# Kernel optimization log

Measured on AMD Instinct MI355X. Metric: run time of the kernel, lower is better.

Reference implementation:

```python
import jax
import jax.numpy as jnp
from jax import lax
import numpy as np

D_MODEL = 768
D_INNER = 1536  # d_model * expand_factor
D_STATE = 16
D_CONV = 4
BATCH = 2
SEQ = 2048
EPS = 1e-5


def silu(x):
    return x * jax.nn.sigmoid(x)


def setup_inputs() -> dict:
    key = jax.random.key(0)
    ks = jax.random.split(key, 24)
    n = lambda k, shape, s=0.1: jax.random.normal(k, shape, dtype=jnp.float32) * s
    inp = {
        "x": jax.random.normal(ks[0], (BATCH, SEQ, D_MODEL), dtype=jnp.float32),
        "ln_g": jnp.ones((D_MODEL,), jnp.float32),
        "ln_b": jnp.zeros((D_MODEL,), jnp.float32),
        "W_in": n(ks[1], (D_INNER, D_MODEL)),
        "b_in": n(ks[2], (D_INNER,)),
        "conv_w": n(ks[3], (D_INNER, 1, D_CONV), 0.02),
        "conv_b": jnp.zeros((D_INNER,), jnp.float32),
        "W_A": n(ks[4], (D_STATE, D_INNER)),
        "b_A": n(ks[5], (D_STATE,)),
        "W_B": n(ks[6], (D_STATE, D_INNER)),
        "b_B": n(ks[7], (D_STATE,)),
        "W_C": n(ks[8], (D_STATE, D_INNER)),
        "b_C": n(ks[9], (D_STATE,)),
        "W_dt": n(ks[10], (D_STATE, D_INNER)),
        "b_dt": n(ks[11], (D_STATE,)),
        "W_S": n(ks[12], (2 * D_INNER, D_INNER)),
        "b_S": n(ks[13], (2 * D_INNER,)),
        "W_gate": n(ks[14], (D_INNER, D_MODEL)),
        "b_gate": n(ks[15], (D_INNER,)),
        "W_out": n(ks[16], (D_MODEL, D_INNER)),
        "b_out": n(ks[17], (D_MODEL,)),
    }
    return inp


def reference(x, ln_g, ln_b, W_in, b_in, conv_w, conv_b, W_A, b_A, W_B, b_B,
              W_C, b_C, W_dt, b_dt, W_S, b_S, W_gate, b_gate, W_out, b_out):
    residual = x
    # LayerNorm
    mu = jnp.mean(x, axis=-1, keepdims=True)
    var = jnp.mean((x - mu) ** 2, axis=-1, keepdims=True)
    xn = (x - mu) * lax.rsqrt(var + EPS) * ln_g + ln_b
    # in projection -> [B, S, D_INNER]
    xp = xn @ W_in.T + b_in
    # depthwise causal conv1d over time
    k = conv_w.shape[-1]
    xc = jnp.moveaxis(xp, 1, 2)  # [B, D, L]
    xc = lax.conv_general_dilated(
        xc, conv_w, window_strides=(1,), padding=[(k - 1, 0)],
        dimension_numbers=("NCH", "OIH", "NCH"),
        feature_group_count=xc.shape[1])
    xc = xc + conv_b[None, :, None]
    xa = silu(jnp.moveaxis(xc, 1, 2))  # [B, S, D]
    # selective gating of SSM input (S_b computed but unused, as in source)
    S = xa @ W_S.T + b_S
    d = xa.shape[-1]
    S_a = jax.nn.sigmoid(S[..., :d])
    u = xa * S_a  # [B, S, D]
    # input-dependent SSM params [B, S, N]
    A = -jnp.exp(u @ W_A.T + b_A)
    dt = jnp.exp(u @ W_dt.T + b_dt)
    Bm = u @ W_B.T + b_B
    Cm = u @ W_C.T + b_C
    decay = jnp.exp(A * dt)  # [B, S, N]

    def step(h, inputs):
        dec_t, B_t, C_t, u_t = inputs  # [B,N],[B,N],[B,N],[B,D]
        h = h * dec_t[:, None, :] + B_t[:, None, :] * u_t[:, :, None]  # [B,D,N]
        y = jnp.einsum("bdn,bn->bd", h, C_t)
        return h, y

    h0 = jnp.zeros((u.shape[0], u.shape[2], decay.shape[-1]), u.dtype)
    scan_in = (jnp.moveaxis(decay, 1, 0), jnp.moveaxis(Bm, 1, 0),
               jnp.moveaxis(Cm, 1, 0), jnp.moveaxis(u, 1, 0))
    _, ys = lax.scan(step, h0, scan_in)
    y = jnp.moveaxis(ys, 0, 1)  # [B, S, D]
    # output gating + projection + residual
    gate = silu(xn @ W_gate.T + b_gate)
    out = (gate * y) @ W_out.T + b_out + residual
    return out
```

## Files before the change

### kernel.cpp

```cpp
#include <hip/hip_runtime.h>


typedef unsigned short u16;
using short8 = __attribute__((ext_vector_type(8))) short;
using f32x4  = __attribute__((ext_vector_type(4))) float;

#define BATCH 2
#define SEQ   2048
#define DM    768
#define DI    1536
#define NIG   (2*DI)
#define NST   16
#define LCH   64
#define NCH   32
#define NTOK  (BATCH*SEQ)

__device__ __forceinline__ u16 f2b(float x) {
  unsigned u = __float_as_uint(x);
  u += 0x7FFFu + ((u >> 16) & 1u);
  return (u16)(u >> 16);
}
__device__ __forceinline__ float b2f(u16 v) { return __uint_as_float((unsigned)v << 16); }
__device__ __forceinline__ float sigmoidf_(float x) { return 1.f / (1.f + expf(-x)); }
__device__ __forceinline__ float siluf_(float x) { return x / (1.f + expf(-x)); }

__global__ __launch_bounds__(256) void cast_bf16(const float* __restrict__ in, u16* __restrict__ out, int n4) {
  int i = blockIdx.x * 256 + threadIdx.x;
  if (i >= n4) return;
  float4 v = ((const float4*)in)[i];
  ushort4 o; o.x = f2b(v.x); o.y = f2b(v.y); o.z = f2b(v.z); o.w = f2b(v.w);
  ((ushort4*)out)[i] = o;
}

__global__ __launch_bounds__(256) void cast_ingate(const float* __restrict__ Wi, const float* __restrict__ Wg,
                                                   const float* __restrict__ bi, const float* __restrict__ bg,
                                                   u16* __restrict__ Wb, float* __restrict__ bias) {
  int i = blockIdx.x * 256 + threadIdx.x;
  if (i >= NIG * DM) return;
  int r = i / DM, c = i % DM;
  Wb[i] = f2b(r < DI ? Wi[(size_t)r * DM + c] : Wg[(size_t)(r - DI) * DM + c]);
  if (i < NIG) bias[i] = (i < DI) ? bi[i] : bg[i - DI];
}

__global__ __launch_bounds__(256) void cast_wabcd(const float* __restrict__ WA, const float* __restrict__ Wdt,
                                                  const float* __restrict__ WB, const float* __restrict__ WC,
                                                  const float* __restrict__ bA, const float* __restrict__ bdt,
                                                  const float* __restrict__ bB, const float* __restrict__ bC,
                                                  u16* __restrict__ Wb, float* __restrict__ bias64) {
  int i = blockIdx.x * 256 + threadIdx.x;
  if (i >= 64 * DI) return;
  int r = i / DI, c = i % DI;
  const float* src = (r < 16) ? WA + (size_t)r * DI
                  : (r < 32) ? Wdt + (size_t)(r - 16) * DI
                  : (r < 48) ? WB + (size_t)(r - 32) * DI
                             : WC + (size_t)(r - 48) * DI;
  Wb[i] = f2b(src[c]);
  if (i < 64) bias64[i] = (i < 16) ? bA[i] : (i < 32) ? bdt[i - 16] : (i < 48) ? bB[i - 32] : bC[i - 48];
}

__global__ __launch_bounds__(256) void ln_kernel(const float* __restrict__ x, const float* __restrict__ g,
                                                 const float* __restrict__ bb, u16* __restrict__ xn) {
  int m = blockIdx.x, tid = threadIdx.x;
  const float* xr = x + (size_t)m * DM;
  float v0 = xr[tid], v1 = xr[tid + 256], v2 = xr[tid + 512];
  float s  = v0 + v1 + v2;
  float s2 = fmaf(v0, v0, fmaf(v1, v1, v2 * v2));
  #pragma unroll
  for (int off = 32; off > 0; off >>= 1) { s += __shfl_down(s, off); s2 += __shfl_down(s2, off); }
  __shared__ float sh[8];
  int wave = tid >> 6, lane = tid & 63;
  if (lane == 0) { sh[wave] = s; sh[4 + wave] = s2; }
  __syncthreads();
  float S1 = sh[0] + sh[1] + sh[2] + sh[3];
  float S2 = sh[4] + sh[5] + sh[6] + sh[7];
  float mu = S1 * (1.f / DM);
  float var = S2 * (1.f / DM) - mu * mu;
  float rs = rsqrtf(var + 1e-5f);
  u16* o = xn + (size_t)m * DM;
  o[tid]       = f2b((v0 - mu) * rs * g[tid]       + bb[tid]);
  o[tid + 256] = f2b((v1 - mu) * rs * g[tid + 256] + bb[tid + 256]);
  o[tid + 512] = f2b((v2 - mu) * rs * g[tid + 512] + bb[tid + 512]);
}

__device__ __forceinline__ void gll16(const void* g, void* l) {
  __builtin_amdgcn_global_load_lds((const __attribute__((address_space(1))) void*)g,
                                   (__attribute__((address_space(3))) void*)l, 16, 0, 0);
}

template <int MODE>
__global__ __launch_bounds__(512) void gemm_bt(const u16* __restrict__ A, const u16* __restrict__ B,
                                               const float* __restrict__ bias, const float* __restrict__ aux,
                                               const u16* __restrict__ auxb,
                                               float* __restrict__ C, u16* __restrict__ Cb,
                                               int M, int N, int K) {
  __shared__ __align__(16) u16 As[4][128 * 32];
  __shared__ __align__(16) u16 Bs[4][128 * 32];
  const int tid = threadIdx.x, wave = tid >> 6, lane = tid & 63;

  const int nbx = gridDim.x, nwg = nbx * gridDim.y;
  const int orig = blockIdx.y * nbx + blockIdx.x;
  const int cpx = nwg >> 3;
  const int swz = (orig & 7) * cpx + (orig >> 3);
  const int m0 = (swz / nbx) * 128, n0 = (swz % nbx) * 128;

  const int wm = (wave >> 1) * 32, wn = (wave & 1) * 64;
  const int fr = lane & 15, fq = lane >> 4;
  f32x4 acc[2][4] = {};

  const int c0 = tid;
  const u16* Ag0 = A + (size_t)(m0 + (c0 >> 2)) * K + ((c0 & 3) ^ ((c0 >> 3) & 3)) * 8;
  const u16* Bg0 = B + (size_t)(n0 + (c0 >> 2)) * K + ((c0 & 3) ^ ((c0 >> 3) & 3)) * 8;
  const int lofs = (wave * 64) * 8;

  int offA[2], offB[4];
  #pragma unroll
  for (int i = 0; i < 2; ++i) {
    int ra = wm + i * 16 + fr;
    offA[i] = ra * 32 + (fq ^ ((ra >> 1) & 3)) * 8;
  }
  #pragma unroll
  for (int i = 0; i < 4; ++i) {
    int rb = wn + i * 16 + fr;
    offB[i] = rb * 32 + (fq ^ ((rb >> 1) & 3)) * 8;
  }

  const int nk = K >> 5;

#define STAGE_BT(tt) { gll16(Ag0 + (tt) * 32, (u16*)As[(tt) & 3] + lofs); \
                       gll16(Bg0 + (tt) * 32, (u16*)Bs[(tt) & 3] + lofs); }
#define COMPUTE_BT(tt) { const u16* as_ = As[(tt) & 3]; const u16* bs_ = Bs[(tt) & 3]; \
    short8 av[2], bv[4]; \
    _Pragma("unroll") for (int i = 0; i < 2; ++i) av[i] = *(const short8*)(as_ + offA[i]); \
    _Pragma("unroll") for (int i = 0; i < 4; ++i) bv[i] = *(const short8*)(bs_ + offB[i]); \
    _Pragma("unroll") for (int mi = 0; mi < 2; ++mi) \
      _Pragma("unroll") for (int ni = 0; ni < 4; ++ni) \
        acc[mi][ni] = __builtin_amdgcn_mfma_f32_16x16x32_bf16(av[mi], bv[ni], acc[mi][ni], 0, 0, 0); }

  STAGE_BT(0); STAGE_BT(1); STAGE_BT(2);

  for (int t = 0; t < nk - 3; ++t) {
    asm volatile("s_waitcnt vmcnt(4)" ::: "memory");
    __builtin_amdgcn_s_barrier();
    STAGE_BT(t + 3);
    COMPUTE_BT(t);
  }
  asm volatile("s_waitcnt vmcnt(4)" ::: "memory");
  __builtin_amdgcn_s_barrier();
  COMPUTE_BT(nk - 3);
  asm volatile("s_waitcnt vmcnt(2)" ::: "memory");
  __builtin_amdgcn_s_barrier();
  COMPUTE_BT(nk - 2);
  asm volatile("s_waitcnt vmcnt(0)" ::: "memory");
  __builtin_amdgcn_s_barrier();
  COMPUTE_BT(nk - 1);
#undef STAGE_BT
#undef COMPUTE_BT

  #pragma unroll
  for (int ni = 0; ni < 4; ++ni) {
    int col = n0 + wn + ni * 16 + fr;
    float bv_ = bias[col];
    #pragma unroll
    for (int mi = 0; mi < 2; ++mi) {
      int row = m0 + wm + mi * 16 + fq * 4;
      #pragma unroll
      for (int j = 0; j < 4; ++j) {
        size_t off = (size_t)(row + j) * N + col;
        float z = acc[mi][ni][j] + bv_;
        if (MODE == 0) {
          C[off] = z + aux[off];
        } else if (MODE == 1) {
          Cb[off] = f2b(b2f(auxb[off]) * sigmoidf_(z));
        } else {
          Cb[off] = f2b(z);
        }
      }
    }
  }
}

__global__ __launch_bounds__(256) void gemm_abcd(const u16* __restrict__ A, const u16* __restrict__ B,
                                                 float* __restrict__ Zp, int M, int K) {
  __shared__ __align__(16) u16 As[2][64 * 64];
  __shared__ __align__(16) u16 Bs[2][64 * 64];
  const int tid = threadIdx.x, wave = tid >> 6, lane = tid & 63;
  const int m0 = blockIdx.x * 64;
  const int ks = blockIdx.y;
  const int Kq = K >> 2;
  const int kbase = ks * Kq;
  const int wm = wave * 16;
  const int fr = lane & 15, fq = lane >> 4;
  f32x4 acc[4] = {};

  const int c0 = tid, c1 = tid + 256;
  const u16* Ag0 = A + (size_t)(m0 + (c0 >> 3)) * K + kbase + ((c0 & 7) ^ ((c0 >> 3) & 7)) * 8;
  const u16* Ag1 = A + (size_t)(m0 + (c1 >> 3)) * K + kbase + ((c1 & 7) ^ ((c1 >> 3) & 7)) * 8;
  const u16* Bg0 = B + (size_t)(c0 >> 3) * K + kbase + ((c0 & 7) ^ ((c0 >> 3) & 7)) * 8;
  const u16* Bg1 = B + (size_t)(c1 >> 3) * K + kbase + ((c1 & 7) ^ ((c1 >> 3) & 7)) * 8;
  const int lo0 = (wave * 64) * 8;
  const int lo1 = (256 + wave * 64) * 8;

  int offAv[2], offBv[2][4];
  {
    int r = wm + fr;
    #pragma unroll
    for (int kk = 0; kk < 2; ++kk) offAv[kk] = r * 64 + ((kk * 4 + fq) ^ (r & 7)) * 8;
    #pragma unroll
    for (int i = 0; i < 4; ++i) {
      int rb = i * 16 + fr;
      #pragma unroll
      for (int kk = 0; kk < 2; ++kk) offBv[kk][i] = rb * 64 + ((kk * 4 + fq) ^ (rb & 7)) * 8;
    }
  }

  const int nk = Kq >> 6;
  gll16(Ag0, (u16*)As[0] + lo0);
  gll16(Ag1, (u16*)As[0] + lo1);
  gll16(Bg0, (u16*)Bs[0] + lo0);
  gll16(Bg1, (u16*)Bs[0] + lo1);

  for (int t = 0; t < nk; ++t) {
    __syncthreads();
    if (t + 1 < nk) {
      int ko = (t + 1) * 64;
      gll16(Ag0 + ko, (u16*)As[(t + 1) & 1] + lo0);
      gll16(Ag1 + ko, (u16*)As[(t + 1) & 1] + lo1);
      gll16(Bg0 + ko, (u16*)Bs[(t + 1) & 1] + lo0);
      gll16(Bg1 + ko, (u16*)Bs[(t + 1) & 1] + lo1);
    }
    const u16* as = As[t & 1];
    const u16* bs = Bs[t & 1];
    #pragma unroll
    for (int kk = 0; kk < 2; ++kk) {
      short8 av = *(const short8*)(as + offAv[kk]);
      short8 bv[4];
      #pragma unroll
      for (int i = 0; i < 4; ++i) bv[i] = *(const short8*)(bs + offBv[kk][i]);
      #pragma unroll
      for (int ni = 0; ni < 4; ++ni)
        acc[ni] = __builtin_amdgcn_mfma_f32_16x16x32_bf16(av, bv[ni], acc[ni], 0, 0, 0);
    }
  }

  float* zp = Zp + (size_t)ks * M * 64;
  #pragma unroll
  for (int ni = 0; ni < 4; ++ni) {
    int col = ni * 16 + fr;
    #pragma unroll
    for (int j = 0; j < 4; ++j) {
      int row = m0 + wm + fq * 4 + j;
      zp[(size_t)row * 64 + col] = acc[ni][j];
    }
  }
}

__global__ __launch_bounds__(256) void abcd_combine(const float* __restrict__ Zp, const float* __restrict__ bias64,
                                                    float* __restrict__ dec, float* __restrict__ Bm,
                                                    float* __restrict__ Cm, int M) {
  int idx = blockIdx.x * 256 + threadIdx.x;
  int row = idx >> 4, n = idx & 15;
  float zA = bias64[n], zDt = bias64[16 + n], zB = bias64[32 + n], zC = bias64[48 + n];
  #pragma unroll
  for (int ks = 0; ks < 4; ++ks) {
    const float* zp = Zp + ((size_t)ks * M + row) * 64;
    zA += zp[n]; zDt += zp[16 + n]; zB += zp[32 + n]; zC += zp[48 + n];
  }
  size_t o = (size_t)row * NST + n;
  dec[o] = expf(-expf(zA + zDt));
  Bm[o] = zB;
  Cm[o] = zC;
}

__global__ __launch_bounds__(256) void conv_silu(const u16* __restrict__ xpg, const float* __restrict__ cw,
                                                 const float* __restrict__ cb, u16* __restrict__ xab) {
  int idx = blockIdx.x * 256 + threadIdx.x;
  int d8 = idx % (DI / 8);
  int token = idx / (DI / 8);
  int t = token % SEQ;
  int d0 = d8 * 8;
  const short8* xv = (const short8*)(xpg + (size_t)token * NIG + d0);
  short8 z8 = {0, 0, 0, 0, 0, 0, 0, 0};
  short8 x3 = (t >= 3) ? xv[-3 * (NIG / 8)] : z8;
  short8 x2 = (t >= 2) ? xv[-2 * (NIG / 8)] : z8;
  short8 x1 = (t >= 1) ? xv[-1 * (NIG / 8)] : z8;
  short8 x0 = xv[0];
  const float4* cw4 = (const float4*)cw;
  float4 cbl = ((const float4*)cb)[d8 * 2], cbh = ((const float4*)cb)[d8 * 2 + 1];
  float cbv[8] = {cbl.x, cbl.y, cbl.z, cbl.w, cbh.x, cbh.y, cbh.z, cbh.w};
  short8 o;
  #pragma unroll
  for (int j = 0; j < 8; ++j) {
    float4 w = cw4[d0 + j];
    float a = cbv[j];
    a = fmaf(b2f((u16)x3[j]), w.x, a);
    a = fmaf(b2f((u16)x2[j]), w.y, a);
    a = fmaf(b2f((u16)x1[j]), w.z, a);
    a = fmaf(b2f((u16)x0[j]), w.w, a);
    o[j] = (short)f2b(siluf_(a));
  }
  *(short8*)(xab + (size_t)token * DI + d0) = o;
}

__global__ __launch_bounds__(256) void scan_phase1(const u16* __restrict__ ub, const float* __restrict__ dec,
                                                   const float* __restrict__ Bm, float* __restrict__ lend,
                                                   float* __restrict__ P) {
  __shared__ float dl[LCH * NST], bl[LCH * NST];
  int bid = blockIdx.x;
  int dblk = bid % 6, b = (bid / 6) % BATCH, c = bid / (6 * BATCH);
  int d = dblk * 256 + threadIdx.x;
  int t0 = c * LCH;
  size_t base16 = (size_t)(b * SEQ + t0) * NST;
  for (int i = threadIdx.x; i < LCH * NST; i += 256) { dl[i] = dec[base16 + i]; bl[i] = Bm[base16 + i]; }
  __syncthreads();
  float h[NST];
  #pragma unroll
  for (int n = 0; n < NST; ++n) h[n] = 0.f;
  const u16* up = ub + (size_t)(b * SEQ + t0) * DI + d;
  for (int t = 0; t < LCH; ++t) {
    float uu = b2f(up[(size_t)t * DI]);
    #pragma unroll
    for (int n = 0; n < NST; ++n) h[n] = fmaf(h[n], dl[t * NST + n], bl[t * NST + n] * uu);
  }
  float* lo = lend + ((size_t)(c * BATCH + b) * DI + d) * NST;
  ((float4*)lo)[0] = make_float4(h[0], h[1], h[2], h[3]);
  ((float4*)lo)[1] = make_float4(h[4], h[5], h[6], h[7]);
  ((float4*)lo)[2] = make_float4(h[8], h[9], h[10], h[11]);
  ((float4*)lo)[3] = make_float4(h[12], h[13], h[14], h[15]);
  if (dblk == 0 && threadIdx.x < NST) {
    float pr = 1.f;
    for (int t = 0; t < LCH; ++t) pr *= dl[t * NST + threadIdx.x];
    P[(size_t)(c * BATCH + b) * NST + threadIdx.x] = pr;
  }
}

__global__ __launch_bounds__(256) void scan_phase2(const float* __restrict__ lend, const float* __restrict__ P,
                                                   float* __restrict__ Hin) {
  int flat = blockIdx.x * 256 + threadIdx.x;
  int n = flat & 15;
  int d = (flat >> 4) % DI;
  int b = flat / (DI * NST);
  float h = 0.f;
  for (int c = 0; c < NCH; ++c) {
    size_t idx = ((size_t)(c * BATCH + b) * DI + d) * NST + n;
    Hin[idx] = h;
    h = fmaf(P[(size_t)(c * BATCH + b) * NST + n], h, lend[idx]);
  }
}

__global__ __launch_bounds__(256) void scan_phase3(const u16* __restrict__ ub, const float* __restrict__ dec,
                                                   const float* __restrict__ Bm, const float* __restrict__ Cm,
                                                   const float* __restrict__ Hin, const u16* __restrict__ xpg,
                                                   u16* __restrict__ gy) {
  __shared__ float dl[LCH * NST], bl[LCH * NST], cl[LCH * NST];
  int bid = blockIdx.x;
  int dblk = bid % 6, b = (bid / 6) % BATCH, c = bid / (6 * BATCH);
  int d = dblk * 256 + threadIdx.x;
  int t0 = c * LCH;
  size_t base16 = (size_t)(b * SEQ + t0) * NST;
  for (int i = threadIdx.x; i < LCH * NST; i += 256) {
    dl[i] = dec[base16 + i]; bl[i] = Bm[base16 + i]; cl[i] = Cm[base16 + i];
  }
  __syncthreads();
  float h[NST];
  const float4* hi = (const float4*)(Hin + ((size_t)(c * BATCH + b) * DI + d) * NST);
  float4 h0 = hi[0], h1 = hi[1], h2 = hi[2], h3 = hi[3];
  h[0]=h0.x; h[1]=h0.y; h[2]=h0.z; h[3]=h0.w; h[4]=h1.x; h[5]=h1.y; h[6]=h1.z; h[7]=h1.w;
  h[8]=h2.x; h[9]=h2.y; h[10]=h2.z; h[11]=h2.w; h[12]=h3.x; h[13]=h3.y; h[14]=h3.z; h[15]=h3.w;
  const u16* up = ub + (size_t)(b * SEQ + t0) * DI + d;
  const u16* gp = xpg + (size_t)(b * SEQ + t0) * NIG + DI + d;
  u16* yp = gy + (size_t)(b * SEQ + t0) * DI + d;
  for (int t = 0; t < LCH; ++t) {
    float uu = b2f(up[(size_t)t * DI]);
    float acc = 0.f;
    #pragma unroll
    for (int n = 0; n < NST; ++n) {
      h[n] = fmaf(h[n], dl[t * NST + n], bl[t * NST + n] * uu);
      acc = fmaf(h[n], cl[t * NST + n], acc);
    }
    float g = b2f(gp[(size_t)t * NIG]);
    yp[(size_t)t * DI] = f2b(siluf_(g) * acc);
  }
}

extern "C" void kernel_launch(void* const* d_in, const int* in_sizes, int n_in,
                              void* d_out, int out_size, void* d_ws, size_t ws_size,
                              hipStream_t stream) {
  const float* x      = (const float*)d_in[0];
  const float* ln_g   = (const float*)d_in[1];
  const float* ln_b   = (const float*)d_in[2];
  const float* W_in   = (const float*)d_in[3];
  const float* b_in   = (const float*)d_in[4];
  const float* conv_w = (const float*)d_in[5];
  const float* conv_b = (const float*)d_in[6];
  const float* W_A    = (const float*)d_in[7];
  const float* b_A    = (const float*)d_in[8];
  const float* W_B    = (const float*)d_in[9];
  const float* b_B    = (const float*)d_in[10];
  const float* W_C    = (const float*)d_in[11];
  const float* b_C    = (const float*)d_in[12];
  const float* W_dt   = (const float*)d_in[13];
  const float* b_dt   = (const float*)d_in[14];
  const float* W_S    = (const float*)d_in[15];
  const float* b_S    = (const float*)d_in[16];
  const float* W_gate = (const float*)d_in[17];
  const float* b_gate = (const float*)d_in[18];
  const float* W_out  = (const float*)d_in[19];
  const float* b_out  = (const float*)d_in[20];
  float* out = (float*)d_out;

  char* p = (char*)d_ws;
  auto alloc = [&](size_t bytes) { char* r = p; p += (bytes + 255) & ~(size_t)255; return r; };
  u16*   Wigb    = (u16*)alloc((size_t)NIG * DM * 2);
  float* biasig  = (float*)alloc((size_t)NIG * 4);
  u16*   WSb     = (u16*)alloc((size_t)DI * DI * 2);
  u16*   Woutb   = (u16*)alloc((size_t)DM * DI * 2);
  u16*   Wabcd   = (u16*)alloc((size_t)64 * DI * 2);
  float* bias64  = (float*)alloc(64 * 4);
  u16*   xnb     = (u16*)alloc((size_t)NTOK * DM * 2);
  u16*   xpg     = (u16*)alloc((size_t)NTOK * NIG * 2);
  u16*   xab     = (u16*)alloc((size_t)NTOK * DI * 2);
  u16*   ub      = (u16*)alloc((size_t)NTOK * DI * 2);
  float* Zp      = (float*)alloc((size_t)4 * NTOK * 64 * 4);
  float* decb    = (float*)alloc((size_t)NTOK * NST * 4);
  float* Bmb     = (float*)alloc((size_t)NTOK * NST * 4);
  float* Cmb     = (float*)alloc((size_t)NTOK * NST * 4);
  float* lend    = (float*)alloc((size_t)NCH * BATCH * DI * NST * 4);
  float* Hin     = (float*)alloc((size_t)NCH * BATCH * DI * NST * 4);
  float* P       = (float*)alloc((size_t)NCH * BATCH * NST * 4);
  u16* gy = xab;

  cast_ingate<<<(NIG * DM + 255) / 256, 256, 0, stream>>>(W_in, W_gate, b_in, b_gate, Wigb, biasig);
  cast_bf16<<<(DI * DI / 4 + 255) / 256, 256, 0, stream>>>(W_S, WSb, DI * DI / 4);
  cast_bf16<<<(DM * DI / 4 + 255) / 256, 256, 0, stream>>>(W_out, Woutb, DM * DI / 4);
  cast_wabcd<<<(64 * DI + 255) / 256, 256, 0, stream>>>(W_A, W_dt, W_B, W_C, b_A, b_dt, b_B, b_C, Wabcd, bias64);

  ln_kernel<<<NTOK, 256, 0, stream>>>(x, ln_g, ln_b, xnb);

  gemm_bt<2><<<dim3(NIG / 128, NTOK / 128), 512, 0, stream>>>(xnb, Wigb, biasig, nullptr, nullptr,
                                                              nullptr, xpg, NTOK, NIG, DM);

  conv_silu<<<NTOK * (DI / 8) / 256, 256, 0, stream>>>(xpg, conv_w, conv_b, xab);

  gemm_bt<1><<<dim3(DI / 128, NTOK / 128), 512, 0, stream>>>(xab, WSb, b_S, nullptr, xab,
                                                             nullptr, ub, NTOK, DI, DI);

  gemm_abcd<<<dim3(NTOK / 64, 4), 256, 0, stream>>>(ub, Wabcd, Zp, NTOK, DI);
  abcd_combine<<<NTOK * 16 / 256, 256, 0, stream>>>(Zp, bias64, decb, Bmb, Cmb, NTOK);

  scan_phase1<<<NCH * BATCH * (DI / 256), 256, 0, stream>>>(ub, decb, Bmb, lend, P);
  scan_phase2<<<BATCH * DI * NST / 256, 256, 0, stream>>>(lend, P, Hin);
  scan_phase3<<<NCH * BATCH * (DI / 256), 256, 0, stream>>>(ub, decb, Bmb, Cmb, Hin, xpg, gy);

  gemm_bt<0><<<dim3(DM / 128, NTOK / 128), 512, 0, stream>>>(gy, Woutb, b_out, x, nullptr,
                                                             out, nullptr, NTOK, DM, DI);
}
```

Before: 206.0 us.

## Use 4-wave GEMM blocks with 64x64 warp tiles and triple buffering

The bf16 GEMM kernel goes from 512 threads with 32x64 per-wave tiles to 256 threads with 64x64 per-wave tiles. Each wave now issues 16 MFMAs per k-step against 8 LDS fragment loads, which raises register reuse. The LDS pipeline drops from four stages to three with rotating buffer indices, and each thread stages two chunks per operand. Two weight cast kernels are also merged into one launch. The cost is more accumulator registers, a shallower prefetch depth, and fewer waves to hide latency.

After: 216.5 us. 5.1% more time.

```diff
diff --git a/kernel.cpp b/kernel.cpp
--- a/kernel.cpp
+++ b/kernel.cpp
@@ -24,12 +24,19 @@
 __device__ __forceinline__ float sigmoidf_(float x) { return 1.f / (1.f + expf(-x)); }
 __device__ __forceinline__ float siluf_(float x) { return x / (1.f + expf(-x)); }
 
-__global__ __launch_bounds__(256) void cast_bf16(const float* __restrict__ in, u16* __restrict__ out, int n4) {
+__global__ __launch_bounds__(256) void cast_two(const float* __restrict__ in1, u16* __restrict__ out1, int n1,
+                                                const float* __restrict__ in2, u16* __restrict__ out2, int n2) {
   int i = blockIdx.x * 256 + threadIdx.x;
-  if (i >= n4) return;
-  float4 v = ((const float4*)in)[i];
-  ushort4 o; o.x = f2b(v.x); o.y = f2b(v.y); o.z = f2b(v.z); o.w = f2b(v.w);
-  ((ushort4*)out)[i] = o;
+  if (i < n1) {
+    float4 v = ((const float4*)in1)[i];
+    ushort4 o; o.x = f2b(v.x); o.y = f2b(v.y); o.z = f2b(v.z); o.w = f2b(v.w);
+    ((ushort4*)out1)[i] = o;
+  } else if (i - n1 < n2) {
+    int j = i - n1;
+    float4 v = ((const float4*)in2)[j];
+    ushort4 o; o.x = f2b(v.x); o.y = f2b(v.y); o.z = f2b(v.z); o.w = f2b(v.w);
+    ((ushort4*)out2)[j] = o;
+  }
 }
 
 __global__ __launch_bounds__(256) void cast_ingate(const float* __restrict__ Wi, const float* __restrict__ Wg,
@@ -88,13 +95,13 @@
 }
 
 template <int MODE>
-__global__ __launch_bounds__(512) void gemm_bt(const u16* __restrict__ A, const u16* __restrict__ B,
+__global__ __launch_bounds__(256) void gemm_bt(const u16* __restrict__ A, const u16* __restrict__ B,
                                                const float* __restrict__ bias, const float* __restrict__ aux,
                                                const u16* __restrict__ auxb,
                                                float* __restrict__ C, u16* __restrict__ Cb,
                                                int M, int N, int K) {
-  __shared__ __align__(16) u16 As[4][128 * 32];
-  __shared__ __align__(16) u16 Bs[4][128 * 32];
+  __shared__ __align__(16) u16 As[3][128 * 32];
+  __shared__ __align__(16) u16 Bs[3][128 * 32];
   const int tid = threadIdx.x, wave = tid >> 6, lane = tid & 63;
 
   const int nbx = gridDim.x, nwg = nbx * gridDim.y;
@@ -103,56 +110,57 @@
   const int swz = (orig & 7) * cpx + (orig >> 3);
   const int m0 = (swz / nbx) * 128, n0 = (swz % nbx) * 128;
 
-  const int wm = (wave >> 1) * 32, wn = (wave & 1) * 64;
+  const int wm = (wave >> 1) * 64, wn = (wave & 1) * 64;
   const int fr = lane & 15, fq = lane >> 4;
-  f32x4 acc[2][4] = {};
-
-  const int c0 = tid;
+  f32x4 acc[4][4] = {};
+
+  const int c0 = tid, c1 = tid + 256;
   const u16* Ag0 = A + (size_t)(m0 + (c0 >> 2)) * K + ((c0 & 3) ^ ((c0 >> 3) & 3)) * 8;
+  const u16* Ag1 = A + (size_t)(m0 + (c1 >> 2)) * K + ((c1 & 3) ^ ((c1 >> 3) & 3)) * 8;
   const u16* Bg0 = B + (size_t)(n0 + (c0 >> 2)) * K + ((c0 & 3) ^ ((c0 >> 3) & 3)) * 8;
-  const int lofs = (wave * 64) * 8;
-
-  int offA[2], offB[4];
-  #pragma unroll
-  for (int i = 0; i < 2; ++i) {
+  const u16* Bg1 = B + (size_t)(n0 + (c1 >> 2)) * K + ((c1 & 3) ^ ((c1 >> 3) & 3)) * 8;
+  const int lo0 = (wave * 64) * 8;
+  const int lo1 = (256 + wave * 64) * 8;
+
+  int offA[4], offB[4];
+  #pragma unroll
+  for (int i = 0; i < 4; ++i) {
     int ra = wm + i * 16 + fr;
+    int rb = wn + i * 16 + fr;
     offA[i] = ra * 32 + (fq ^ ((ra >> 1) & 3)) * 8;
-  }
-  #pragma unroll
-  for (int i = 0; i < 4; ++i) {
-    int rb = wn + i * 16 + fr;
     offB[i] = rb * 32 + (fq ^ ((rb >> 1) & 3)) * 8;
   }
 
   const int nk = K >> 5;
 
-#define STAGE_BT(tt) { gll16(Ag0 + (tt) * 32, (u16*)As[(tt) & 3] + lofs); \
-                       gll16(Bg0 + (tt) * 32, (u16*)Bs[(tt) & 3] + lofs); }
-#define COMPUTE_BT(tt) { const u16* as_ = As[(tt) & 3]; const u16* bs_ = Bs[(tt) & 3]; \
-    short8 av[2], bv[4]; \
-    _Pragma("unroll") for (int i = 0; i < 2; ++i) av[i] = *(const short8*)(as_ + offA[i]); \
+#define STAGE_BT(tt, bb) { gll16(Ag0 + (tt) * 32, (u16*)As[bb] + lo0); \
+                           gll16(Ag1 + (tt) * 32, (u16*)As[bb] + lo1); \
+                           gll16(Bg0 + (tt) * 32, (u16*)Bs[bb] + lo0); \
+                           gll16(Bg1 + (tt) * 32, (u16*)Bs[bb] + lo1); }
+#define COMPUTE_BT(bb) { const u16* as_ = As[bb]; const u16* bs_ = Bs[bb]; \
+    short8 av[4], bv[4]; \
+    _Pragma("unroll") for (int i = 0; i < 4; ++i) av[i] = *(const short8*)(as_ + offA[i]); \
     _Pragma("unroll") for (int i = 0; i < 4; ++i) bv[i] = *(const short8*)(bs_ + offB[i]); \
-    _Pragma("unroll") for (int mi = 0; mi < 2; ++mi) \
+    _Pragma("unroll") for (int mi = 0; mi < 4; ++mi) \
       _Pragma("unroll") for (int ni = 0; ni < 4; ++ni) \
         acc[mi][ni] = __builtin_amdgcn_mfma_f32_16x16x32_bf16(av[mi], bv[ni], acc[mi][ni], 0, 0, 0); }
 
-  STAGE_BT(0); STAGE_BT(1); STAGE_BT(2);
-
-  for (int t = 0; t < nk - 3; ++t) {
+  STAGE_BT(0, 0); STAGE_BT(1, 1);
+  int b0 = 0, b1 = 1, b2 = 2;
+
+  for (int t = 0; t < nk - 2; ++t) {
     asm volatile("s_waitcnt vmcnt(4)" ::: "memory");
     __builtin_amdgcn_s_barrier();
-    STAGE_BT(t + 3);
-    COMPUTE_BT(t);
+    STAGE_BT(t + 2, b2);
+    COMPUTE_BT(b0);
+    int tmp = b0; b0 = b1; b1 = b2; b2 = tmp;
   }
   asm volatile("s_waitcnt vmcnt(4)" ::: "memory");
   __builtin_amdgcn_s_barrier();
-  COMPUTE_BT(nk - 3);
-  asm volatile("s_waitcnt vmcnt(2)" ::: "memory");
-  __builtin_amdgcn_s_barrier();
-  COMPUTE_BT(nk - 2);
+  COMPUTE_BT(b0);
   asm volatile("s_waitcnt vmcnt(0)" ::: "memory");
   __builtin_amdgcn_s_barrier();
-  COMPUTE_BT(nk - 1);
+  COMPUTE_BT(b1);
 #undef STAGE_BT
 #undef COMPUTE_BT
 
@@ -161,7 +169,7 @@
     int col = n0 + wn + ni * 16 + fr;
     float bv_ = bias[col];
     #pragma unroll
-    for (int mi = 0; mi < 2; ++mi) {
+    for (int mi = 0; mi < 4; ++mi) {
       int row = m0 + wm + mi * 16 + fq * 4;
       #pragma unroll
       for (int j = 0; j < 4; ++j) {
@@ -430,18 +438,18 @@
   u16* gy = xab;
 
   cast_ingate<<<(NIG * DM + 255) / 256, 256, 0, stream>>>(W_in, W_gate, b_in, b_gate, Wigb, biasig);
-  cast_bf16<<<(DI * DI / 4 + 255) / 256, 256, 0, stream>>>(W_S, WSb, DI * DI / 4);
-  cast_bf16<<<(DM * DI / 4 + 255) / 256, 256, 0, stream>>>(W_out, Woutb, DM * DI / 4);
+  cast_two<<<(DI * DI / 4 + DM * DI / 4 + 255) / 256, 256, 0, stream>>>(W_S, WSb, DI * DI / 4,
+                                                                        W_out, Woutb, DM * DI / 4);
   cast_wabcd<<<(64 * DI + 255) / 256, 256, 0, stream>>>(W_A, W_dt, W_B, W_C, b_A, b_dt, b_B, b_C, Wabcd, bias64);
 
   ln_kernel<<<NTOK, 256, 0, stream>>>(x, ln_g, ln_b, xnb);
 
-  gemm_bt<2><<<dim3(NIG / 128, NTOK / 128), 512, 0, stream>>>(xnb, Wigb, biasig, nullptr, nullptr,
+  gemm_bt<2><<<dim3(NIG / 128, NTOK / 128), 256, 0, stream>>>(xnb, Wigb, biasig, nullptr, nullptr,
                                                               nullptr, xpg, NTOK, NIG, DM);
 
   conv_silu<<<NTOK * (DI / 8) / 256, 256, 0, stream>>>(xpg, conv_w, conv_b, xab);
 
-  gemm_bt<1><<<dim3(DI / 128, NTOK / 128), 512, 0, stream>>>(xab, WSb, b_S, nullptr, xab,
+  gemm_bt<1><<<dim3(DI / 128, NTOK / 128), 256, 0, stream>>>(xab, WSb, b_S, nullptr, xab,
                                                              nullptr, ub, NTOK, DI, DI);
 
   gemm_abcd<<<dim3(NTOK / 64, 4), 256, 0, stream>>>(ub, Wabcd, Zp, NTOK, DI);
@@ -451,6 +459,6 @@
   scan_phase2<<<BATCH * DI * NST / 256, 256, 0, stream>>>(lend, P, Hin);
   scan_phase3<<<NCH * BATCH * (DI / 256), 256, 0, stream>>>(ub, decb, Bmb, Cmb, Hin, xpg, gy);
 
-  gemm_bt<0><<<dim3(DM / 128, NTOK / 128), 512, 0, stream>>>(gy, Woutb, b_out, x, nullptr,
+  gemm_bt<0><<<dim3(DM / 128, NTOK / 128), 256, 0, stream>>>(gy, Woutb, b_out, x, nullptr,
                                                              out, nullptr, NTOK, DM, DI);
 }
```

## Use 256x256-tile GEMM for input/gate projection and merge weight cast kernels

Applied to the files above, without the earlier changes.

Replaces the 128x128-tile GEMM for the fused input+gate projection with a new 256x256-tile kernel. It uses a K-step of 64, double-buffered LDS staging split across phases, and s_setprio around the MFMA blocks. The aim is more data reuse per tile and fewer global loads. The existing GEMM also gets setprio hints, and the two bf16 weight casts are merged into one launch to save launch overhead. The trade-offs: the grid for this GEMM drops to 12x16=192 workgroups, which may underfill the CUs, and the larger tile uses 128KB of LDS per workgroup and raises register pressure.

Result: slower. 211.7 us (+2.8%).

```diff
diff --git a/kernel.cpp b/kernel.cpp
--- a/kernel.cpp
+++ b/kernel.cpp
@@ -24,12 +24,19 @@
 __device__ __forceinline__ float sigmoidf_(float x) { return 1.f / (1.f + expf(-x)); }
 __device__ __forceinline__ float siluf_(float x) { return x / (1.f + expf(-x)); }
 
-__global__ __launch_bounds__(256) void cast_bf16(const float* __restrict__ in, u16* __restrict__ out, int n4) {
+__global__ __launch_bounds__(256) void cast_two(const float* __restrict__ in1, u16* __restrict__ out1, int n1,
+                                                const float* __restrict__ in2, u16* __restrict__ out2, int n2) {
   int i = blockIdx.x * 256 + threadIdx.x;
-  if (i >= n4) return;
-  float4 v = ((const float4*)in)[i];
-  ushort4 o; o.x = f2b(v.x); o.y = f2b(v.y); o.z = f2b(v.z); o.w = f2b(v.w);
-  ((ushort4*)out)[i] = o;
+  if (i < n1) {
+    float4 v = ((const float4*)in1)[i];
+    ushort4 o; o.x = f2b(v.x); o.y = f2b(v.y); o.z = f2b(v.z); o.w = f2b(v.w);
+    ((ushort4*)out1)[i] = o;
+  } else if (i - n1 < n2) {
+    int j = i - n1;
+    float4 v = ((const float4*)in2)[j];
+    ushort4 o; o.x = f2b(v.x); o.y = f2b(v.y); o.z = f2b(v.z); o.w = f2b(v.w);
+    ((ushort4*)out2)[j] = o;
+  }
 }
 
 __global__ __launch_bounds__(256) void cast_ingate(const float* __restrict__ Wi, const float* __restrict__ Wg,
@@ -87,6 +94,92 @@
                                    (__attribute__((address_space(3))) void*)l, 16, 0, 0);
 }
 
+__global__ __launch_bounds__(512) void gemm256(const u16* __restrict__ A, const u16* __restrict__ B,
+                                               const float* __restrict__ bias, u16* __restrict__ Cb,
+                                               int M, int N, int K) {
+  __shared__ __align__(16) u16 As[2][256 * 64];
+  __shared__ __align__(16) u16 Bs[2][256 * 64];
+  const int tid = threadIdx.x, wave = tid >> 6, lane = tid & 63;
+
+  const int nbx = gridDim.x, nwg = nbx * gridDim.y;
+  const int orig = blockIdx.y * nbx + blockIdx.x;
+  const int cpx = nwg >> 3;
+  const int swz = (orig & 7) * cpx + (orig >> 3);
+  const int m0 = (swz / nbx) * 256, n0 = (swz % nbx) * 256;
+
+  const int wm = (wave >> 2) * 128, wn = (wave & 3) * 64;
+  const int fr = lane & 15, fq = lane >> 4;
+  f32x4 acc[8][4] = {};
+
+  const int strow = tid >> 3;
+  const int gk8 = ((tid & 7) ^ (strow & 7)) * 8;
+  const u16* Ags = A + (size_t)(m0 + strow) * K + gk8;
+  const u16* Bgs = B + (size_t)(n0 + strow) * K + gk8;
+  const int ldst = wave * 512;
+
+  int offA[2][8], offB[2][4];
+  #pragma unroll
+  for (int ks = 0; ks < 2; ++ks) {
+    #pragma unroll
+    for (int i = 0; i < 8; ++i)
+      offA[ks][i] = (wm + i * 16 + fr) * 64 + (((ks * 4 + fq) ^ (fr & 7))) * 8;
+    #pragma unroll
+    for (int j = 0; j < 4; ++j)
+      offB[ks][j] = (wn + j * 16 + fr) * 64 + (((ks * 4 + fq) ^ (fr & 7))) * 8;
+  }
+
+#define STG256(kt, s, bb) { \
+    gll16(Ags + (size_t)(s) * 64 * K + (size_t)(kt) * 64, (u16*)As[bb] + (s) * 4096 + ldst); \
+    gll16(Bgs + (size_t)(s) * 64 * K + (size_t)(kt) * 64, (u16*)Bs[bb] + (s) * 4096 + ldst); }
+#define PH256(as_, bs_, ks, mh) { \
+    short8 av[4], bv[4]; \
+    _Pragma("unroll") for (int i = 0; i < 4; ++i) av[i] = *(const short8*)((as_) + offA[ks][(mh) * 4 + i]); \
+    _Pragma("unroll") for (int j = 0; j < 4; ++j) bv[j] = *(const short8*)((bs_) + offB[ks][j]); \
+    __builtin_amdgcn_s_setprio(1); \
+    _Pragma("unroll") for (int i = 0; i < 4; ++i) \
+      _Pragma("unroll") for (int j = 0; j < 4; ++j) \
+        acc[(mh) * 4 + i][j] = __builtin_amdgcn_mfma_f32_16x16x32_bf16(av[i], bv[j], acc[(mh) * 4 + i][j], 0, 0, 0); \
+    __builtin_amdgcn_s_setprio(0); }
+
+  const int nt = K >> 6;
+  STG256(0, 0, 0); STG256(0, 1, 0); STG256(0, 2, 0); STG256(0, 3, 0);
+
+  for (int t = 0; t < nt; ++t) {
+    const int cur = t & 1, nxt = cur ^ 1;
+    const bool pf = (t + 1 < nt);
+    asm volatile("s_waitcnt vmcnt(0)" ::: "memory");
+    __builtin_amdgcn_s_barrier();
+    const u16* as = As[cur]; const u16* bs = Bs[cur];
+    if (pf) { STG256(t + 1, 0, nxt); STG256(t + 1, 1, nxt); }
+    PH256(as, bs, 0, 0);
+    __builtin_amdgcn_s_barrier();
+    if (pf) STG256(t + 1, 2, nxt);
+    PH256(as, bs, 0, 1);
+    __builtin_amdgcn_s_barrier();
+    if (pf) STG256(t + 1, 3, nxt);
+    PH256(as, bs, 1, 0);
+    __builtin_amdgcn_s_barrier();
+    PH256(as, bs, 1, 1);
+  }
+#undef STG256
+#undef PH256
+
+  #pragma unroll
+  for (int ni = 0; ni < 4; ++ni) {
+    int col = n0 + wn + ni * 16 + fr;
+    float bv_ = bias[col];
+    #pragma unroll
+    for (int mi = 0; mi < 8; ++mi) {
+      int row = m0 + wm + mi * 16 + fq * 4;
+      #pragma unroll
+      for (int j = 0; j < 4; ++j) {
+        size_t off = (size_t)(row + j) * N + col;
+        Cb[off] = f2b(acc[mi][ni][j] + bv_);
+      }
+    }
+  }
+}
+
 template <int MODE>
 __global__ __launch_bounds__(512) void gemm_bt(const u16* __restrict__ A, const u16* __restrict__ B,
                                                const float* __restrict__ bias, const float* __restrict__ aux,
@@ -132,9 +225,11 @@
     short8 av[2], bv[4]; \
     _Pragma("unroll") for (int i = 0; i < 2; ++i) av[i] = *(const short8*)(as_ + offA[i]); \
     _Pragma("unroll") for (int i = 0; i < 4; ++i) bv[i] = *(const short8*)(bs_ + offB[i]); \
+    __builtin_amdgcn_s_setprio(1); \
     _Pragma("unroll") for (int mi = 0; mi < 2; ++mi) \
       _Pragma("unroll") for (int ni = 0; ni < 4; ++ni) \
-        acc[mi][ni] = __builtin_amdgcn_mfma_f32_16x16x32_bf16(av[mi], bv[ni], acc[mi][ni], 0, 0, 0); }
+        acc[mi][ni] = __builtin_amdgcn_mfma_f32_16x16x32_bf16(av[mi], bv[ni], acc[mi][ni], 0, 0, 0); \
+    __builtin_amdgcn_s_setprio(0); }
 
   STAGE_BT(0); STAGE_BT(1); STAGE_BT(2);
 
@@ -169,10 +264,8 @@
         float z = acc[mi][ni][j] + bv_;
         if (MODE == 0) {
           C[off] = z + aux[off];
-        } else if (MODE == 1) {
+        } else {
           Cb[off] = f2b(b2f(auxb[off]) * sigmoidf_(z));
-        } else {
-          Cb[off] = f2b(z);
         }
       }
     }
@@ -430,14 +523,13 @@
   u16* gy = xab;
 
   cast_ingate<<<(NIG * DM + 255) / 256, 256, 0, stream>>>(W_in, W_gate, b_in, b_gate, Wigb, biasig);
-  cast_bf16<<<(DI * DI / 4 + 255) / 256, 256, 0, stream>>>(W_S, WSb, DI * DI / 4);
-  cast_bf16<<<(DM * DI / 4 + 255) / 256, 256, 0, stream>>>(W_out, Woutb, DM * DI / 4);
+  cast_two<<<(DI * DI / 4 + DM * DI / 4 + 255) / 256, 256, 0, stream>>>(W_S, WSb, DI * DI / 4,
+                                                                        W_out, Woutb, DM * DI / 4);
   cast_wabcd<<<(64 * DI + 255) / 256, 256, 0, stream>>>(W_A, W_dt, W_B, W_C, b_A, b_dt, b_B, b_C, Wabcd, bias64);
 
   ln_kernel<<<NTOK, 256, 0, stream>>>(x, ln_g, ln_b, xnb);
 
-  gemm_bt<2><<<dim3(NIG / 128, NTOK / 128), 512, 0, stream>>>(xnb, Wigb, biasig, nullptr, nullptr,
-                                                              nullptr, xpg, NTOK, NIG, DM);
+  gemm256<<<dim3(NIG / 256, NTOK / 256), 512, 0, stream>>>(xnb, Wigb, biasig, xpg, NTOK, NIG, DM);
 
   conv_silu<<<NTOK * (DI / 8) / 256, 256, 0, stream>>>(xpg, conv_w, conv_b, xab);
 
```
